# Kernel optimization log

Measured on AMD Instinct MI355X. Metric: run time of the kernel, lower is better.

Reference implementation:

```python
import jax, jax.numpy as jnp
import numpy as np

B, T, D, H = 8, 512, 1024, 16
DK = D // H  # 64
EPS = 1e-3  # Keras BatchNormalization default epsilon


def batchnorm(x, gamma, beta):
    # Keras BN over feature axis (-1), training-mode batch statistics over (B, T)
    mean = jnp.mean(x, axis=(0, 1), keepdims=True)
    var = jnp.var(x, axis=(0, 1), keepdims=True)
    return (x - mean) * jax.lax.rsqrt(var + EPS) * gamma + beta


def setup_inputs() -> dict:
    key = jax.random.key(0)
    ks = jax.random.split(key, 12)
    s = 0.05
    return {
        "x": jax.random.normal(ks[0], (B, T, D), dtype=jnp.float32),
        "Wq": jax.random.uniform(ks[1], (H, D, DK), dtype=jnp.float32, minval=-s, maxval=s),
        "Wk": jax.random.uniform(ks[2], (H, D, DK), dtype=jnp.float32, minval=-s, maxval=s),
        "Wv": jax.random.uniform(ks[3], (H, D, DK), dtype=jnp.float32, minval=-s, maxval=s),
        "W": jax.random.uniform(ks[4], (D, D), dtype=jnp.float32, minval=-s, maxval=s),
        "W1": jax.random.normal(ks[5], (D, D), dtype=jnp.float32) * 0.02,
        "b1": jnp.zeros((D,), dtype=jnp.float32),
        "W2": jax.random.normal(ks[6], (D, D), dtype=jnp.float32) * 0.02,
        "b2": jnp.zeros((D,), dtype=jnp.float32),
        "g1": jnp.ones((D,), dtype=jnp.float32),
        "be1": jnp.zeros((D,), dtype=jnp.float32),
        "g2": jnp.ones((D,), dtype=jnp.float32),
        "be2": jnp.zeros((D,), dtype=jnp.float32),
    }


def reference(x, Wq, Wk, Wv, W, W1, b1, W2, b2, g1, be1, g2, be2):
    # Batched multi-head attention (replaces the per-head Python loop)
    q = jnp.einsum("btd,hdk->bhtk", x, Wq)
    k = jnp.einsum("btd,hdk->bhtk", x, Wk)
    v = jnp.einsum("btd,hdk->bhtk", x, Wv)
    scores = jnp.einsum("bhtk,bhsk->bhts", q, k) / jnp.sqrt(jnp.float32(DK))
    w = jax.nn.softmax(scores, axis=-1)
    attn = jnp.einsum("bhts,bhsk->bhtk", w, v)
    # concat heads: [B,H,T,DK] -> [B,T,H*DK] (head-major concat order as in the loop)
    concat = jnp.transpose(attn, (0, 2, 1, 3)).reshape(B, T, D)
    out = concat @ W
    out1 = batchnorm(x + out, g1, be1)
    out2 = jax.nn.relu(out1 @ W1 + b1) @ W2 + b2
    return batchnorm(out1 + out2, g2, be2)
```

## Files before the change

### kernel.cpp

```cpp
#include <hip/hip_runtime.h>
#include <hip/hip_bf16.h>
#include <cstdint>

#define Bn 8
#define Tn 512
#define Dn 1024
#define Hn 16
#define DKn 64
#define Mn (Bn * Tn)

typedef unsigned short u16;
typedef short bf16x8 __attribute__((ext_vector_type(8)));
typedef float f32x4 __attribute__((ext_vector_type(4)));

__device__ __forceinline__ u16 f2bf(float f) {
  unsigned int u = __builtin_bit_cast(unsigned int, f);
  u += 0x7fffu + ((u >> 16) & 1u);
  return (u16)(u >> 16);
}
__device__ __forceinline__ unsigned int pack2bf(float lo, float hi) {
  return (unsigned int)f2bf(lo) | ((unsigned int)f2bf(hi) << 16);
}

__device__ __forceinline__ void gl2lds16(const void* g, void* l) {
  __builtin_amdgcn_global_load_lds(
      (const __attribute__((address_space(1))) unsigned int*)g,
      (__attribute__((address_space(3))) unsigned int*)l,
      16, 0, 0);
}

__global__ __launch_bounds__(256) void cvt_bf16_k(
    const float* __restrict__ src, u16* __restrict__ dst)
{
  const size_t i = ((size_t)blockIdx.x * 256 + threadIdx.x) * 8;
  float4 a = *reinterpret_cast<const float4*>(&src[i]);
  float4 b = *reinterpret_cast<const float4*>(&src[i + 4]);
  uint4 w;
  w.x = pack2bf(a.x, a.y); w.y = pack2bf(a.z, a.w);
  w.z = pack2bf(b.x, b.y); w.w = pack2bf(b.z, b.w);
  *reinterpret_cast<uint4*>(&dst[i]) = w;
}

__global__ __launch_bounds__(256) void tqkv_k(
    const float* __restrict__ wq, const float* __restrict__ wk,
    const float* __restrict__ wv, u16* __restrict__ dst)
{
  const int kt = blockIdx.x;
  const int y  = blockIdx.y;
  const int tau = y >> 4, head = y & 15;
  const float* src = (tau == 0 ? wq : tau == 1 ? wk : wv) + (size_t)head * 65536;
  const int t = threadIdx.x;
  const int n  = t & 63;
  const int kq = (t >> 6) << 4;
  const int k0 = kt << 6;
  u16 v[16];
#pragma unroll
  for (int j = 0; j < 16; j++)
    v[j] = f2bf(src[(size_t)(k0 + kq + j) * 64 + n]);
  u16* d = &dst[((size_t)tau * 1024 + head * 64 + n) * 1024 + k0 + kq];
  *reinterpret_cast<uint4*>(&d[0]) = *reinterpret_cast<uint4*>(&v[0]);
  *reinterpret_cast<uint4*>(&d[8]) = *reinterpret_cast<uint4*>(&v[8]);
}

__global__ __launch_bounds__(256) void tw_k(
    const float* __restrict__ W, const float* __restrict__ W1,
    const float* __restrict__ W2, u16* __restrict__ wt,
    u16* __restrict__ w1t, u16* __restrict__ w2t)
{
  const int kt = blockIdx.x, ntl = blockIdx.y, z = blockIdx.z;
  const float* src = (z == 0 ? W : z == 1 ? W1 : W2);
  u16* dst = (z == 0 ? wt : z == 1 ? w1t : w2t);
  const int t = threadIdx.x;
  const int n  = (ntl << 6) + (t & 63);
  const int kq = (t >> 6) << 4;
  const int k0 = kt << 6;
  u16 v[16];
#pragma unroll
  for (int j = 0; j < 16; j++)
    v[j] = f2bf(src[(size_t)(k0 + kq + j) * 1024 + n]);
  u16* d = &dst[(size_t)n * 1024 + k0 + kq];
  *reinterpret_cast<uint4*>(&d[0]) = *reinterpret_cast<uint4*>(&v[0]);
  *reinterpret_cast<uint4*>(&d[8]) = *reinterpret_cast<uint4*>(&v[8]);
}

template<int BIAS, int RELU, int OUTM, int RES, int VT, int RESNORM>
__global__ __launch_bounds__(512) void mgemm_k(
    const u16* __restrict__ A, const u16* __restrict__ Bt,
    const float* __restrict__ bias,
    float* __restrict__ Cf, u16* __restrict__ Cb, int ldc,
    const float* __restrict__ Rres, float* __restrict__ Rout,
    float* __restrict__ psum, float* __restrict__ psumsq,
    u16* __restrict__ Vt,
    const float* __restrict__ nsc, const float* __restrict__ nsh)
{
  __shared__ __align__(16) u16 As[2][4096];
  __shared__ __align__(16) u16 Bs[2][4096];

  const int nwg = gridDim.x * gridDim.y;
  const int fid = blockIdx.y * gridDim.x + blockIdx.x;
  const int lid = (fid & 7) * (nwg >> 3) + (fid >> 3);
  const int bx = lid % gridDim.x, by = lid / gridDim.x;

  const int tid  = threadIdx.x;
  const int lane = tid & 63;
  const int wid  = tid >> 6;
  const int wm = wid >> 2, wn = wid & 3;
  const int g4 = lane >> 4, r15 = lane & 15;
  const int m0 = by << 7, n0 = bx << 7;

  const int srow  = tid >> 2;
  const int sslot = tid & 3;
  const int ssw   = (srow ^ (srow >> 2)) & 3;
  const int sk8   = ((sslot ^ ssw) << 3);
  const u16* ga0 = &A[(size_t)(m0 + srow) * 1024 + sk8];
  const u16* gb0 = &Bt[(size_t)(n0 + srow) * 1024 + sk8];
  const int lofs = wid * 1024;

  f32x4 acc[4][2] = {};

  gl2lds16(ga0, (char*)As[0] + lofs);
  gl2lds16(gb0, (char*)Bs[0] + lofs);
  __syncthreads();

#pragma unroll 1
  for (int t = 0; t < 32; t++) {
    const int cur = t & 1;
    if (t < 31) {
      gl2lds16(ga0 + (t + 1) * 32, (char*)As[cur ^ 1] + lofs);
      gl2lds16(gb0 + (t + 1) * 32, (char*)Bs[cur ^ 1] + lofs);
    }
    bf16x8 af[4], bfr[2];
#pragma unroll
    for (int m = 0; m < 4; m++) {
      int row = wm * 64 + m * 16 + r15;
      int sw = (row ^ (row >> 2)) & 3;
      af[m] = *reinterpret_cast<const bf16x8*>(
          (const char*)As[cur] + row * 64 + ((g4 ^ sw) << 4));
    }
#pragma unroll
    for (int n = 0; n < 2; n++) {
      int row = wn * 32 + n * 16 + r15;
      int sw = (row ^ (row >> 2)) & 3;
      bfr[n] = *reinterpret_cast<const bf16x8*>(
          (const char*)Bs[cur] + row * 64 + ((g4 ^ sw) << 4));
    }
#pragma unroll
    for (int m = 0; m < 4; m++)
#pragma unroll
      for (int n = 0; n < 2; n++)
        acc[m][n] = __builtin_amdgcn_mfma_f32_16x16x32_bf16(af[m], bfr[n], acc[m][n], 0, 0, 0);
    __syncthreads();
  }

  if (VT && bx >= 16) {
    const int vcol0 = n0 - 2048;
#pragma unroll
    for (int m = 0; m < 4; m++) {
      int row0 = m0 + wm * 64 + m * 16 + g4 * 4;
      int bI = row0 >> 9, s = row0 & 511;
#pragma unroll
      for (int n = 0; n < 2; n++) {
        int cv = vcol0 + wn * 32 + n * 16 + r15;
        int hh = cv >> 6, dk = cv & 63;
        uint2 pk;
        pk.x = pack2bf(acc[m][n][0], acc[m][n][1]);
        pk.y = pack2bf(acc[m][n][2], acc[m][n][3]);
        *reinterpret_cast<uint2*>(
            &Vt[(((size_t)(bI * 16 + hh) * 64 + dk) << 9) + s]) = pk;
      }
    }
    return;
  }

  float bb[2] = {0.f, 0.f};
  if (BIAS) {
#pragma unroll
    for (int n = 0; n < 2; n++) bb[n] = bias[n0 + wn * 32 + n * 16 + r15];
  }

  if (RES) {
    float sc_[2], sh_[2];
    if (RESNORM) {
#pragma unroll
      for (int n = 0; n < 2; n++) {
        int col = n0 + wn * 32 + n * 16 + r15;
        sc_[n] = nsc[col];
        sh_[n] = nsh[col];
      }
    }
    float sp[2] = {0.f, 0.f}, sq[2] = {0.f, 0.f};
#pragma unroll
    for (int m = 0; m < 4; m++) {
      int row = m0 + wm * 64 + m * 16 + g4 * 4;
#pragma unroll
      for (int n = 0; n < 2; n++) {
        int col = n0 + wn * 32 + n * 16 + r15;
#pragma unroll
        for (int j = 0; j < 4; j++) {
          float v = acc[m][n][j] + bb[n];
          float res = Rres[(size_t)(row + j) * 1024 + col];
          if (RESNORM) res = fmaf(res, sc_[n], sh_[n]);
          float r = v + res;
          Rout[(size_t)(row + j) * 1024 + col] = r;
          sp[n] += r;
          sq[n] = fmaf(r, r, sq[n]);
        }
      }
    }
#pragma unroll
    for (int n = 0; n < 2; n++) {
      sp[n] += __shfl_xor(sp[n], 16, 64);
      sp[n] += __shfl_xor(sp[n], 32, 64);
      sq[n] += __shfl_xor(sq[n], 16, 64);
      sq[n] += __shfl_xor(sq[n], 32, 64);
    }
    if (g4 == 0) {
      int slot = (by << 1) + wm;
#pragma unroll
      for (int n = 0; n < 2; n++) {
        int col = n0 + wn * 32 + n * 16 + r15;
        psum[(size_t)slot * 1024 + col] = sp[n];
        psumsq[(size_t)slot * 1024 + col] = sq[n];
      }
    }
    return;
  }

#pragma unroll
  for (int m = 0; m < 4; m++) {
    int row = m0 + wm * 64 + m * 16 + g4 * 4;
#pragma unroll
    for (int n = 0; n < 2; n++) {
      int col = n0 + wn * 32 + n * 16 + r15;
#pragma unroll
      for (int j = 0; j < 4; j++) {
        float v = acc[m][n][j];
        if (BIAS) v += bb[n];
        if (RELU) v = fmaxf(v, 0.f);
        if (OUTM == 1)      Cb[(size_t)(row + j) * ldc + col] = f2bf(v);
        else if (OUTM == 0) Cf[(size_t)(row + j) * ldc + col] = v;
      }
    }
  }
}

__global__ __launch_bounds__(256, 2) void attn_k(
    const u16* __restrict__ qk, const u16* __restrict__ Vt,
    u16* __restrict__ o)
{
  __shared__ __align__(16) unsigned char Ks[2][16384];
  __shared__ __align__(16) unsigned char Vs[2][16384];
  __shared__ __align__(16) unsigned char Ps[16384];

  const int bh  = blockIdx.x;
  const int qc  = blockIdx.y;
  const int b   = bh >> 4, h = bh & 15;
  const int tid = threadIdx.x;
  const int lane = tid & 63;
  const int wv   = tid >> 6;
  const int qcol = lane & 15;
  const int g    = lane >> 4;

  const size_t rowbase = (size_t)b * Tn;
  const size_t qrow0   = rowbase + qc * 64 + wv * 16;

  bf16x8 qf[2];
  {
    const u16* qp = &qk[(qrow0 + qcol) * 2048 + h * 64 + g * 8];
    qf[0] = *reinterpret_cast<const bf16x8*>(qp);
    qf[1] = *reinterpret_cast<const bf16x8*>(qp + 32);
  }

  f32x4 oa[4] = {};
  float m_run = -3e38f, l_run = 0.f;

  const int krow = tid >> 3, kch = tid & 7;
  const int vrow = tid >> 4, vch = tid & 15;
  unsigned char* Pw = &Ps[wv * 4096];

#define STAGE_KV(c_, buf_)                                                     \
  {                                                                            \
    _Pragma("unroll")                                                          \
    for (int i = 0; i < 4; i++) {                                              \
      int row = i * 32 + krow;                                                 \
      const u16* gk = &qk[(rowbase + (c_) * 128 + row) * 2048 + 1024 + h * 64  \
                          + ((kch ^ (row & 7)) << 3)];                         \
      gl2lds16(gk, (char*)Ks[buf_] + wv * 1024 + i * 4096);                    \
    }                                                                          \
    _Pragma("unroll")                                                          \
    for (int i = 0; i < 4; i++) {                                              \
      int row = i * 16 + vrow;                                                 \
      const u16* gv = &Vt[(((size_t)bh * 64 + row) << 9) + (c_) * 128          \
                          + ((vch ^ (row & 7)) << 3)];                         \
      gl2lds16(gv, (char*)Vs[buf_] + wv * 1024 + i * 4096);                    \
    }                                                                          \
  }

  STAGE_KV(0, 0);
  __syncthreads();

#pragma unroll 1
  for (int c = 0; c < 4; c++) {
    const int cur = c & 1;
    if (c < 3) STAGE_KV(c + 1, cur ^ 1);

    f32x4 sf[8];
#pragma unroll
    for (int t = 0; t < 8; t++) {
      sf[t] = (f32x4){0.f, 0.f, 0.f, 0.f};
      const int srow = t * 16 + qcol;
      const int base = srow * 128;
      const int sw = srow & 7;
#pragma unroll
      for (int ks = 0; ks < 2; ks++) {
        bf16x8 a = *reinterpret_cast<const bf16x8*>(
            &Ks[cur][base + (((ks * 4 + g) ^ sw) << 4)]);
        sf[t] = __builtin_amdgcn_mfma_f32_16x16x32_bf16(a, qf[ks], sf[t], 0, 0, 0);
      }
    }

    float mc = -3e38f;
#pragma unroll
    for (int t = 0; t < 8; t++)
#pragma unroll
      for (int r = 0; r < 4; r++) {
        float s = sf[t][r] * 0.125f;
        sf[t][r] = s;
        mc = fmaxf(mc, s);
      }
    mc = fmaxf(mc, __shfl_xor(mc, 16, 64));
    mc = fmaxf(mc, __shfl_xor(mc, 32, 64));
    float mnew = fmaxf(m_run, mc);
    float alpha = __expf(m_run - mnew);
    m_run = mnew;

    float lsum = 0.f;
#pragma unroll
    for (int t = 0; t < 8; t++)
#pragma unroll
      for (int r = 0; r < 4; r++) {
        float e = __expf(sf[t][r] - mnew);
        sf[t][r] = e;
        lsum += e;
      }
    lsum += __shfl_xor(lsum, 16, 64);
    lsum += __shfl_xor(lsum, 32, 64);
    l_run = l_run * alpha + lsum;

#pragma unroll
    for (int j = 0; j < 4; j++) {
      float av = __shfl(alpha, (g << 4) + g * 4 + j, 64);
#pragma unroll
      for (int nt = 0; nt < 4; nt++) oa[nt][j] *= av;
    }

#pragma unroll
    for (int t = 0; t < 8; t++) {
      int o0 = t * 32 + g * 8;
      int chunk = o0 >> 4;
      int sb = ((chunk ^ (qcol & 7)) << 4) | (o0 & 15);
      *reinterpret_cast<unsigned int*>(&Pw[qcol * 256 + sb]) =
          pack2bf(sf[t][0], sf[t][1]);
      *reinterpret_cast<unsigned int*>(&Pw[qcol * 256 + sb + 4]) =
          pack2bf(sf[t][2], sf[t][3]);
    }

    bf16x8 pa[4];
#pragma unroll
    for (int ks = 0; ks < 4; ks++)
      pa[ks] = *reinterpret_cast<const bf16x8*>(
          &Pw[qcol * 256 + (((ks * 4 + g) ^ (qcol & 7)) << 4)]);
#pragma unroll
    for (int nt = 0; nt < 4; nt++) {
      const int vr = nt * 16 + qcol;
      const int vsw = vr & 7;
#pragma unroll
      for (int ks = 0; ks < 4; ks++) {
        bf16x8 bvf = *reinterpret_cast<const bf16x8*>(
            &Vs[cur][vr * 256 + (((ks * 4 + g) ^ vsw) << 4)]);
        oa[nt] = __builtin_amdgcn_mfma_f32_16x16x32_bf16(pa[ks], bvf, oa[nt], 0, 0, 0);
      }
    }
    __syncthreads();
  }

  float rl = 1.f / l_run;
#pragma unroll
  for (int j = 0; j < 4; j++) {
    float il = __shfl(rl, (g << 4) + g * 4 + j, 64);
#pragma unroll
    for (int nt = 0; nt < 4; nt++)
      o[(qrow0 + g * 4 + j) * 1024 + h * 64 + nt * 16 + qcol] =
          f2bf(oa[nt][j] * il);
  }
#undef STAGE_KV
}

__global__ __launch_bounds__(256) void reduce_stats_k(
    const float* __restrict__ ps, const float* __restrict__ pq,
    const float* __restrict__ g, const float* __restrict__ be,
    float* __restrict__ scale, float* __restrict__ shift)
{
  const int col = blockIdx.x * 256 + threadIdx.x;
  float s = 0.f, q = 0.f;
  for (int p = 0; p < 64; p++) {
    s += ps[(size_t)p * Dn + col];
    q += pq[(size_t)p * Dn + col];
  }
  const float invn = 1.f / 4096.f;
  float mean = s * invn;
  float var = q * invn - mean * mean;
  float inv = rsqrtf(var + 1e-3f);
  float sc = g[col] * inv;
  scale[col] = sc;
  shift[col] = be[col] - mean * sc;
}

template<int OUTMODE>
__global__ __launch_bounds__(256) void norm_k(
    const float* __restrict__ r, const float* __restrict__ scale,
    const float* __restrict__ shift, float* __restrict__ o, u16* __restrict__ ob)
{
  const size_t idx = (size_t)blockIdx.x * 256 + threadIdx.x;
  const int c4 = ((int)idx & 255) << 2;
  float4 rv = *reinterpret_cast<const float4*>(&r[idx << 2]);
  float4 sc = *reinterpret_cast<const float4*>(&scale[c4]);
  float4 sh = *reinterpret_cast<const float4*>(&shift[c4]);
  float4 ov = make_float4(fmaf(rv.x, sc.x, sh.x), fmaf(rv.y, sc.y, sh.y),
                          fmaf(rv.z, sc.z, sh.z), fmaf(rv.w, sc.w, sh.w));
  if (OUTMODE == 0) {
    *reinterpret_cast<float4*>(&o[idx << 2]) = ov;
  } else {
    uint2 p;
    p.x = pack2bf(ov.x, ov.y);
    p.y = pack2bf(ov.z, ov.w);
    *reinterpret_cast<uint2*>(&ob[idx << 2]) = p;
  }
}

extern "C" void kernel_launch(void* const* d_in, const int* in_sizes, int n_in,
                              void* d_out, int out_size, void* d_ws, size_t ws_size,
                              hipStream_t stream)
{
  const float* x   = (const float*)d_in[0];
  const float* wq  = (const float*)d_in[1];
  const float* wk  = (const float*)d_in[2];
  const float* wv  = (const float*)d_in[3];
  const float* W   = (const float*)d_in[4];
  const float* W1  = (const float*)d_in[5];
  const float* b1  = (const float*)d_in[6];
  const float* W2  = (const float*)d_in[7];
  const float* b2  = (const float*)d_in[8];
  const float* g1  = (const float*)d_in[9];
  const float* be1 = (const float*)d_in[10];
  const float* g2  = (const float*)d_in[11];
  const float* be2 = (const float*)d_in[12];

  float* out = (float*)d_out;
  float* ws  = (float*)d_ws;

  const size_t NB = (size_t)Mn * Dn;
  float* ws1    = ws;
  float* ws2    = ws1 + NB;
  float* psum   = ws2 + NB;
  float* psumsq = psum + 64 * Dn;
  float* scale1 = psumsq + 64 * Dn;
  float* shift1 = scale1 + Dn;
  float* scale2 = shift1 + Dn;
  float* shift2 = scale2 + Dn;
  u16* xb      = (u16*)(shift2 + Dn);
  u16* qkb     = xb + NB;
  u16* vtb     = qkb + 2 * NB;
  u16* concatb = vtb + NB;
  u16* wqkvT   = concatb + NB;
  u16* wt      = wqkvT + 3 * 1048576;
  u16* w1t     = wt + 1048576;
  u16* w2t     = w1t + 1048576;
  u16* out1b = qkb;
  u16* hb    = qkb + NB;

  dim3 b256(256), b512(512);

  cvt_bf16_k<<<dim3(2048), b256, 0, stream>>>(x, xb);
  tqkv_k<<<dim3(16, 48), b256, 0, stream>>>(wq, wk, wv, wqkvT);
  tw_k<<<dim3(16, 16, 3), b256, 0, stream>>>(W, W1, W2, wt, w1t, w2t);

  mgemm_k<0, 0, 1, 0, 1, 0><<<dim3(24, 32), b512, 0, stream>>>(
      xb, wqkvT, nullptr, nullptr, qkb, 2048,
      nullptr, nullptr, nullptr, nullptr, vtb, nullptr, nullptr);
  attn_k<<<dim3(128, 8), b256, 0, stream>>>(qkb, vtb, concatb);
  mgemm_k<0, 0, 2, 1, 0, 0><<<dim3(8, 32), b512, 0, stream>>>(
      concatb, wt, nullptr, nullptr, nullptr, 1024,
      x, ws1, psum, psumsq, nullptr, nullptr, nullptr);
  reduce_stats_k<<<dim3(4), b256, 0, stream>>>(psum, psumsq, g1, be1, scale1, shift1);
  norm_k<2><<<dim3(NB / 1024), b256, 0, stream>>>(ws1, scale1, shift1, nullptr, out1b);
  mgemm_k<1, 1, 1, 0, 0, 0><<<dim3(8, 32), b512, 0, stream>>>(
      out1b, w1t, b1, nullptr, hb, 1024,
      nullptr, nullptr, nullptr, nullptr, nullptr, nullptr, nullptr);
  mgemm_k<1, 0, 2, 1, 0, 1><<<dim3(8, 32), b512, 0, stream>>>(
      hb, w2t, b2, nullptr, nullptr, 1024,
      ws1, ws2, psum, psumsq, nullptr, scale1, shift1);
  reduce_stats_k<<<dim3(4), b256, 0, stream>>>(psum, psumsq, g2, be2, scale2, shift2);
  norm_k<0><<<dim3(NB / 1024), b256, 0, stream>>>(ws2, scale2, shift2, out, nullptr);
}
```

Measured before the change: 174.8 us.

## Triple-buffer GEMM LDS staging and use counted vmcnt waits in attention

The GEMM main loop moves from double to triple buffering of the A/B LDS tiles, keeping two tiles in flight. It replaces full __syncthreads drains with an explicit s_waitcnt vmcnt plus a raw s_barrier fenced by sched_barrier. The attention kernel gets the same counted-wait barrier scheme, so the prefetch of the next K/V chunk stays outstanding while the current chunk is computed. The aim is better overlap of global-to-LDS loads with MFMA work, at the cost of 1.5x GEMM LDS usage (possible occupancy loss) and correctness that now depends on hand-counted vmcnt values.

```diff
diff --git a/kernel.cpp b/kernel.cpp
--- a/kernel.cpp
+++ b/kernel.cpp
@@ -28,6 +28,13 @@
       (__attribute__((address_space(3))) unsigned int*)l,
       16, 0, 0);
 }
+
+__device__ __forceinline__ void hard_barrier() {
+  __builtin_amdgcn_sched_barrier(0);
+  __builtin_amdgcn_s_barrier();
+  __builtin_amdgcn_sched_barrier(0);
+}
+#define WAITV(n_) asm volatile("s_waitcnt vmcnt(" #n_ ")" ::: "memory")
 
 __global__ __launch_bounds__(256) void cvt_bf16_k(
     const float* __restrict__ src, u16* __restrict__ dst)
@@ -93,8 +100,8 @@
     u16* __restrict__ Vt,
     const float* __restrict__ nsc, const float* __restrict__ nsh)
 {
-  __shared__ __align__(16) u16 As[2][4096];
-  __shared__ __align__(16) u16 Bs[2][4096];
+  __shared__ __align__(16) u16 As[3][4096];
+  __shared__ __align__(16) u16 Bs[3][4096];
 
   const int nwg = gridDim.x * gridDim.y;
   const int fid = blockIdx.y * gridDim.x + blockIdx.x;
@@ -118,39 +125,54 @@
 
   f32x4 acc[4][2] = {};
 
-  gl2lds16(ga0, (char*)As[0] + lofs);
-  gl2lds16(gb0, (char*)Bs[0] + lofs);
-  __syncthreads();
-
-#pragma unroll 1
-  for (int t = 0; t < 32; t++) {
-    const int cur = t & 1;
-    if (t < 31) {
-      gl2lds16(ga0 + (t + 1) * 32, (char*)As[cur ^ 1] + lofs);
-      gl2lds16(gb0 + (t + 1) * 32, (char*)Bs[cur ^ 1] + lofs);
-    }
+  auto stage_t = [&](int t, int bofs) {
+    gl2lds16(ga0 + t * 32, (char*)As + bofs + lofs);
+    gl2lds16(gb0 + t * 32, (char*)Bs + bofs + lofs);
+  };
+  auto compute_t = [&](int bofs) {
     bf16x8 af[4], bfr[2];
 #pragma unroll
     for (int m = 0; m < 4; m++) {
       int row = wm * 64 + m * 16 + r15;
       int sw = (row ^ (row >> 2)) & 3;
       af[m] = *reinterpret_cast<const bf16x8*>(
-          (const char*)As[cur] + row * 64 + ((g4 ^ sw) << 4));
+          (const char*)As + bofs + row * 64 + ((g4 ^ sw) << 4));
     }
 #pragma unroll
     for (int n = 0; n < 2; n++) {
       int row = wn * 32 + n * 16 + r15;
       int sw = (row ^ (row >> 2)) & 3;
       bfr[n] = *reinterpret_cast<const bf16x8*>(
-          (const char*)Bs[cur] + row * 64 + ((g4 ^ sw) << 4));
+          (const char*)Bs + bofs + row * 64 + ((g4 ^ sw) << 4));
     }
 #pragma unroll
     for (int m = 0; m < 4; m++)
 #pragma unroll
       for (int n = 0; n < 2; n++)
         acc[m][n] = __builtin_amdgcn_mfma_f32_16x16x32_bf16(af[m], bfr[n], acc[m][n], 0, 0, 0);
-    __syncthreads();
-  }
+  };
+
+  stage_t(0, 0);
+  stage_t(1, 8192);
+
+  int rd = 0, wr = 2;
+#pragma unroll 1
+  for (int t = 0; t < 30; ++t) {
+    stage_t(t + 2, wr * 8192);
+    WAITV(4);
+    hard_barrier();
+    compute_t(rd * 8192);
+    hard_barrier();
+    wr = rd;
+    rd = (rd + 1 == 3) ? 0 : rd + 1;
+  }
+  WAITV(2);
+  hard_barrier();
+  compute_t(0);
+  hard_barrier();
+  WAITV(0);
+  hard_barrier();
+  compute_t(8192);
 
   if (VT && bx >= 16) {
     const int vcol0 = n0 - 2048;
@@ -278,32 +300,24 @@
   const int vrow = tid >> 4, vch = tid & 15;
   unsigned char* Pw = &Ps[wv * 4096];
 
-#define STAGE_KV(c_, buf_)                                                     \
-  {                                                                            \
-    _Pragma("unroll")                                                          \
-    for (int i = 0; i < 4; i++) {                                              \
-      int row = i * 32 + krow;                                                 \
-      const u16* gk = &qk[(rowbase + (c_) * 128 + row) * 2048 + 1024 + h * 64  \
-                          + ((kch ^ (row & 7)) << 3)];                         \
-      gl2lds16(gk, (char*)Ks[buf_] + wv * 1024 + i * 4096);                    \
-    }                                                                          \
-    _Pragma("unroll")                                                          \
-    for (int i = 0; i < 4; i++) {                                              \
-      int row = i * 16 + vrow;                                                 \
-      const u16* gv = &Vt[(((size_t)bh * 64 + row) << 9) + (c_) * 128          \
-                          + ((vch ^ (row & 7)) << 3)];                         \
-      gl2lds16(gv, (char*)Vs[buf_] + wv * 1024 + i * 4096);                    \
-    }                                                                          \
-  }
-
-  STAGE_KV(0, 0);
-  __syncthreads();
-
-#pragma unroll 1
-  for (int c = 0; c < 4; c++) {
-    const int cur = c & 1;
-    if (c < 3) STAGE_KV(c + 1, cur ^ 1);
-
+  auto stage_kv = [&](int c, int buf) {
+#pragma unroll
+    for (int i = 0; i < 4; i++) {
+      int row = i * 32 + krow;
+      const u16* gk = &qk[(rowbase + c * 128 + row) * 2048 + 1024 + h * 64
+                          + ((kch ^ (row & 7)) << 3)];
+      gl2lds16(gk, (char*)Ks[buf] + wv * 1024 + i * 4096);
+    }
+#pragma unroll
+    for (int i = 0; i < 4; i++) {
+      int row = i * 16 + vrow;
+      const u16* gv = &Vt[(((size_t)bh * 64 + row) << 9) + c * 128
+                          + ((vch ^ (row & 7)) << 3)];
+      gl2lds16(gv, (char*)Vs[buf] + wv * 1024 + i * 4096);
+    }
+  };
+
+  auto compute_c = [&](int cur) {
     f32x4 sf[8];
 #pragma unroll
     for (int t = 0; t < 8; t++) {
@@ -381,8 +395,20 @@
         oa[nt] = __builtin_amdgcn_mfma_f32_16x16x32_bf16(pa[ks], bvf, oa[nt], 0, 0, 0);
       }
     }
-    __syncthreads();
-  }
+  };
+
+  stage_kv(0, 0);
+#pragma unroll 1
+  for (int c = 0; c < 3; ++c) {
+    stage_kv(c + 1, (c + 1) & 1);
+    WAITV(8);
+    hard_barrier();
+    compute_c(c & 1);
+    hard_barrier();
+  }
+  WAITV(0);
+  hard_barrier();
+  compute_c(1);
 
   float rl = 1.f / l_run;
 #pragma unroll
@@ -393,7 +419,6 @@
       o[(qrow0 + g * 4 + j) * 1024 + h * 64 + nt * 16 + qcol] =
           f2bf(oa[nt][j] * il);
   }
-#undef STAGE_KV
 }
 
 __global__ __launch_bounds__(256) void reduce_stats_k(
```

Measured after the change: 171.9 us. Within noise of the previous version (-1.7%).
